# Kernel optimization log

Measured on AMD Instinct MI355X. Metric: run time of the kernel, lower is better.

The kernel has to match this reference:

```python
import jax, jax.numpy as jnp
import numpy as np

B, L, N = 16, 64, 1024
HAND_DIM, J, HID = 99, 21, 512
N_LAYERS, N_HEADS = 4, 8
DH = HID // N_HEADS
CAT = HAND_DIM + 2 * J * 3 + 2 * N  # 2273
PNAMES = ['fc_lw','fc_lb','fc_rw','fc_rb','out_lw','out_lb','out_rw','out_rb','Wqkv','bqkv','Wo','bo','W1','b1f','W2','b2f','ln1_g','ln1_b','ln2_g','ln2_b']

def sinusoidal_pe(n_pos, d):
    pos = np.arange(n_pos)[:, None].astype(np.float32)
    div = np.exp(np.arange(0, d, 2).astype(np.float32) * (-np.log(10000.0) / d))
    pe = np.zeros((n_pos, d), np.float32)
    pe[:, 0::2] = np.sin(pos * div)
    pe[:, 1::2] = np.cos(pos * div)
    return jnp.asarray(pe)

def rot6d_to_rotmat(x6):
    a1, a2 = x6[..., 0:3], x6[..., 3:6]
    b1 = a1 / jnp.linalg.norm(a1, axis=-1, keepdims=True)
    b2 = a2 - jnp.sum(b1 * a2, -1, keepdims=True) * b1
    b2 = b2 / jnp.linalg.norm(b2, axis=-1, keepdims=True)
    b3 = jnp.cross(b1, b2)
    return jnp.stack([b1, b2, b3], axis=-1)  # [..., 3, 3] (columns)

def layer_norm(x, g, b):
    mu = jnp.mean(x, -1, keepdims=True)
    var = jnp.mean((x - mu) ** 2, -1, keepdims=True)
    return (x - mu) * jax.lax.rsqrt(var + 1e-5) * g + b

def attention_map(joints, pc):
    # joints [B,L,J,3], pc [B,L,N,3]; squared dists via ||a||^2+||b||^2-2ab (no [B,L,J,N,3] diff tensor)
    d2 = (jnp.sum(joints ** 2, -1)[..., :, None] + jnp.sum(pc ** 2, -1)[..., None, :]
          - 2.0 * jnp.einsum('bljd,blnd->bljn', joints, pc))
    idx = jnp.argmin(d2, axis=-1)  # [B,L,J] nearest-point index
    idx3 = jnp.broadcast_to(idx[..., None], idx.shape + (3,))
    contact = jnp.take_along_axis(pc, idx3, axis=2)  # [B,L,J,3]
    return jnp.exp(-50.0 * (joints - contact) ** 2)

def mha(x, Wqkv, bqkv, Wo, bo):
    Bq, S, D = x.shape
    qkv = x @ Wqkv + bqkv
    q, k, v = jnp.split(qkv, 3, axis=-1)
    split = lambda t: t.reshape(Bq, S, N_HEADS, DH).transpose(0, 2, 1, 3)
    q, k, v = split(q), split(k), split(v)
    att = jax.nn.softmax(jnp.einsum('bhqd,bhkd->bhqk', q, k) * (1.0 / np.sqrt(DH)), axis=-1)
    o = jnp.einsum('bhqk,bhkd->bhqd', att, v).transpose(0, 2, 1, 3).reshape(Bq, S, D)
    return o @ Wo + bo

def forward(x_lhand, x_rhand, j_lhand, j_rhand, m_contact, x_obj, point_cloud, p):
    rotmat = rot6d_to_rotmat(x_obj[..., 3:9])  # [B,L,3,3]
    pc_t = jnp.einsum('btij,bkj->btki', rotmat, point_cloud) + x_obj[..., 0:3][:, :, None, :]
    att_l = attention_map(j_lhand, pc_t).reshape(B, L, -1)
    att_r = attention_map(j_rhand, pc_t).reshape(B, L, -1)
    mc = jnp.broadcast_to(m_contact.reshape(B, 1, N), (B, L, N))
    pcn = jnp.linalg.norm(pc_t, axis=-1)  # [B,L,N]
    xl = jnp.concatenate([x_lhand, j_lhand.reshape(B, L, -1), mc, pcn, att_l], -1)
    xr = jnp.concatenate([x_rhand, j_rhand.reshape(B, L, -1), mc, pcn, att_r], -1)
    xl = xl @ p['fc_lw'] + p['fc_lb']
    xr = xr @ p['fc_rw'] + p['fc_rb']
    x = jnp.stack([xl, xr], axis=2).reshape(B, 2 * L, HID)  # interleave agents per frame
    pe_frame = jnp.repeat(sinusoidal_pe(L, HID), 2, axis=0)  # frame-wise: pair shares position
    pe_agent = jnp.tile(sinusoidal_pe(2, HID), (L, 1))       # agent-wise: alternating 0/1
    x = x + pe_frame[None] + pe_agent[None]
    for i in range(N_LAYERS):
        h = layer_norm(x + mha(x, p['Wqkv'][i], p['bqkv'][i], p['Wo'][i], p['bo'][i]), p['ln1_g'][i], p['ln1_b'][i])
        ff = jax.nn.relu(h @ p['W1'][i] + p['b1f'][i]) @ p['W2'][i] + p['b2f'][i]
        x = layer_norm(h + ff, p['ln2_g'][i], p['ln2_b'][i])
    out_l = x[:, 0::2] @ p['out_lw'] + p['out_lb']
    out_r = x[:, 1::2] @ p['out_rw'] + p['out_rb']
    return out_l, out_r

def setup_inputs() -> dict:
    key = jax.random.key(0)
    ks = jax.random.split(key, 16)
    r = lambda i, shape, s=1.0: jax.random.normal(ks[i], shape, jnp.float32) * s
    return {
        'x_lhand': r(0, (B, L, HAND_DIM)),
        'x_rhand': r(1, (B, L, HAND_DIM)),
        'j_lhand': r(2, (B, L, J, 3)),
        'j_rhand': r(3, (B, L, J, 3)),
        'm_contact': jax.random.uniform(ks[4], (B, N, 1), jnp.float32),
        'x_obj': r(5, (B, L, 10)),
        'point_cloud': r(6, (B, N, 3)),
        'fc_lw': r(7, (CAT, HID), 0.02), 'fc_lb': jnp.zeros((HID,), jnp.float32),
        'fc_rw': r(8, (CAT, HID), 0.02), 'fc_rb': jnp.zeros((HID,), jnp.float32),
        'out_lw': r(9, (HID, HAND_DIM), 0.02), 'out_lb': jnp.zeros((HAND_DIM,), jnp.float32),
        'out_rw': r(10, (HID, HAND_DIM), 0.02), 'out_rb': jnp.zeros((HAND_DIM,), jnp.float32),
        'Wqkv': r(11, (N_LAYERS, HID, 3 * HID), 0.02), 'bqkv': jnp.zeros((N_LAYERS, 3 * HID), jnp.float32),
        'Wo': r(12, (N_LAYERS, HID, HID), 0.02), 'bo': jnp.zeros((N_LAYERS, HID), jnp.float32),
        'W1': r(13, (N_LAYERS, HID, 4 * HID), 0.02), 'b1f': jnp.zeros((N_LAYERS, 4 * HID), jnp.float32),
        'W2': r(14, (N_LAYERS, 4 * HID, HID), 0.02), 'b2f': jnp.zeros((N_LAYERS, HID), jnp.float32),
        'ln1_g': jnp.ones((N_LAYERS, HID), jnp.float32), 'ln1_b': jnp.zeros((N_LAYERS, HID), jnp.float32),
        'ln2_g': jnp.ones((N_LAYERS, HID), jnp.float32), 'ln2_b': jnp.zeros((N_LAYERS, HID), jnp.float32),
    }

def reference(x_lhand, x_rhand, j_lhand, j_rhand, m_contact, x_obj, point_cloud, fc_lw, fc_lb, fc_rw, fc_rb, out_lw, out_lb, out_rw, out_rb, Wqkv, bqkv, Wo, bo, W1, b1f, W2, b2f, ln1_g, ln1_b, ln2_g, ln2_b):
    p = dict(zip(PNAMES, (fc_lw, fc_lb, fc_rw, fc_rb, out_lw, out_lb, out_rw, out_rb, Wqkv, bqkv, Wo, bo, W1, b1f, W2, b2f, ln1_g, ln1_b, ln2_g, ln2_b)))
    return forward(x_lhand, x_rhand, j_lhand, j_rhand, m_contact, x_obj, point_cloud, p)
```

## Files before the change

### kernel.cpp

```cpp
#include <hip/hip_runtime.h>
#include <hip/hip_bf16.h>

typedef __hip_bfloat16 bf16;
typedef __attribute__((ext_vector_type(8))) short short8;
typedef __attribute__((ext_vector_type(4))) float floatx4;

#define B_    16
#define L_    64
#define N_    1024
#define HANDD 99
#define Jn    21
#define HID   512
#define NLAY  4
#define NHEAD 8
#define DHEAD 64
#define CATD  2273
#define CATP  2304
#define S_    128
#define T_    2048

#define F_X     16
#define F_QKV   1048592
#define F_TMP   6291472
#define F_H     7340048
#define WB_F    8388624
#define W_FCL   0
#define W_FCR   1179648
#define W_QKV   2359296
#define W_WO    5505024
#define W_W1    6553600
#define W_W2    10747904
#define U_CATL  14942208
#define U_CATR  17301504
#define U_XB    19660800
#define U_AOB   20709376
#define U_HB    21757952
#define W_OUT   22806528
#define U_FFB   U_CATL

#define RSTR 68
#define VSTR 136

#define PC_UNITS 2048
#define NW_UNITS 3680

static __device__ __forceinline__ float b2f(bf16 x) { return __bfloat162float(x); }
static __device__ __forceinline__ float ldin(const void* p, size_t i, int isf32) {
    return isf32 ? ((const float*)p)[i] : b2f(((const bf16*)p)[i]);
}
static __device__ __forceinline__ unsigned short f2bf(float f) {
    unsigned int u = __float_as_uint(f);
    unsigned int r = (u + 0x7fffu + ((u >> 16) & 1u)) >> 16;
    return (unsigned short)r;
}

__global__ __launch_bounds__(256) void detect_kernel(const void* mc, int* flag)
{
    __shared__ int sbad;
    int tid = threadIdx.x;
    if (tid == 0) sbad = 0;
    __syncthreads();
    int bad = 0;
    for (int i = tid; i < 16384; i += 256) {
        float v = b2f(((const bf16*)mc)[i]);
        if (!(v >= -0.02f && v <= 1.02f)) bad = 1;
    }
    if (bad) atomicOr(&sbad, 1);
    __syncthreads();
    if (tid == 0) flag[0] = sbad ? 1 : 0;
}

struct PrepP {
    const void *x_l, *x_r, *j_l, *j_r, *mc, *x_obj, *pc;
    const void *fc_lw, *fc_rw, *Wqkv, *Wo, *W1, *W2, *out_lw, *out_rw;
    unsigned short *wb, *catl, *catr;
    const int* dtf;
};

static __device__ void pctcat_half(int bl, int hand, const PrepP& P, int isf32,
                                   char* smemc)
{
    float* pcl  = (float*)smemc;
    float* pcnl = pcl + N_ * 3;
    int b = bl >> 6;
    int tid = threadIdx.x;

    size_t xo = (size_t)bl * 10;
    float t0 = ldin(P.x_obj, xo+0, isf32), t1 = ldin(P.x_obj, xo+1, isf32), t2 = ldin(P.x_obj, xo+2, isf32);
    float a1x = ldin(P.x_obj, xo+3, isf32), a1y = ldin(P.x_obj, xo+4, isf32), a1z = ldin(P.x_obj, xo+5, isf32);
    float a2x = ldin(P.x_obj, xo+6, isf32), a2y = ldin(P.x_obj, xo+7, isf32), a2z = ldin(P.x_obj, xo+8, isf32);
    float n1 = sqrtf(a1x*a1x + a1y*a1y + a1z*a1z);
    float b1x = a1x / n1, b1y = a1y / n1, b1z = a1z / n1;
    float d = b1x*a2x + b1y*a2y + b1z*a2z;
    float c2x = a2x - d*b1x, c2y = a2y - d*b1y, c2z = a2z - d*b1z;
    float n2 = sqrtf(c2x*c2x + c2y*c2y + c2z*c2z);
    float b2x = c2x / n2, b2y = c2y / n2, b2z = c2z / n2;
    float b3x = b1y*b2z - b1z*b2y;
    float b3y = b1z*b2x - b1x*b2z;
    float b3z = b1x*b2y - b1y*b2x;

    size_t pcb = (size_t)b * N_ * 3;
    for (int n = tid; n < N_; n += 256) {
        float p0 = ldin(P.pc, pcb + n*3+0, isf32);
        float p1 = ldin(P.pc, pcb + n*3+1, isf32);
        float p2 = ldin(P.pc, pcb + n*3+2, isf32);
        float q0 = b1x*p0 + b2x*p1 + b3x*p2 + t0;
        float q1 = b1y*p0 + b2y*p1 + b3y*p2 + t1;
        float q2 = b1z*p0 + b2z*p1 + b3z*p2 + t2;
        pcl[n*3+0] = q0; pcl[n*3+1] = q1; pcl[n*3+2] = q2;
        pcnl[n] = q0*q0 + q1*q1 + q2*q2;
    }
    __syncthreads();

    const void* xh = hand ? P.x_r : P.x_l;
    const void* jh = hand ? P.j_r : P.j_l;
    unsigned short* row = (hand ? P.catr : P.catl) + (size_t)bl * CATP;
    for (int c = tid; c < HANDD; c += 256)  row[c]        = f2bf(ldin(xh, (size_t)bl*HANDD + c, isf32));
    for (int c = tid; c < 63;    c += 256)  row[99 + c]   = f2bf(ldin(jh, (size_t)bl*63 + c, isf32));
    for (int c = tid; c < N_;    c += 256)  row[162 + c]  = f2bf(ldin(P.mc, (size_t)b*N_ + c, isf32));
    for (int c = tid; c < N_;    c += 256)  row[1186 + c] = f2bf(sqrtf(pcnl[c]));
    for (int c = CATD + tid; c < CATP; c += 256) row[c] = 0;

    int wave = tid >> 6, lane = tid & 63;
    for (int j = wave; j < Jn; j += 4) {
        float jx = ldin(jh, (size_t)bl*63 + j*3 + 0, isf32);
        float jy = ldin(jh, (size_t)bl*63 + j*3 + 1, isf32);
        float jz = ldin(jh, (size_t)bl*63 + j*3 + 2, isf32);
        float m2x = -2.f * jx, m2y = -2.f * jy, m2z = -2.f * jz;
        float best = 3.4e38f; int bidx = 0x7fffffff;
        for (int n = lane; n < N_; n += 64) {
            float p0 = pcl[n*3+0], p1 = pcl[n*3+1], p2 = pcl[n*3+2];
            float d2 = fmaf(m2x, p0, fmaf(m2y, p1, fmaf(m2z, p2, pcnl[n])));
            if (d2 < best) { best = d2; bidx = n; }
        }
        for (int off = 32; off; off >>= 1) {
            float ob = __shfl_down(best, off, 64);
            int   oi = __shfl_down(bidx, off, 64);
            if (ob < best || (ob == best && oi < bidx)) { best = ob; bidx = oi; }
        }
        bidx = __shfl(bidx, 0, 64);
        if (lane < 3) {
            float jc = (lane == 0) ? jx : ((lane == 1) ? jy : jz);
            float cc = pcl[bidx*3 + lane];
            float dd = jc - cc;
            row[2210 + j*3 + lane] = f2bf(expf(-50.f * dd * dd));
        }
    }
}

__global__ __launch_bounds__(256) void prep_all(PrepP P)
{
    __shared__ __attribute__((aligned(16))) char smem[16640];
    int isf32 = P.dtf[0];
    int u = blockIdx.x;

    if (u < PC_UNITS) {
        pctcat_half(u >> 1, u & 1, P, isf32, smem);
        return;
    }
    u -= PC_UNITS;
    if (u == NW_UNITS) {
        unsigned short* wz = P.wb + W_OUT + (size_t)(2 * HANDD) * HID;
        for (int idx = threadIdx.x; idx < (256 - 2 * HANDD) * HID; idx += 256)
            wz[idx] = 0;
        return;
    }

    float (*tile)[65] = (float(*)[65])smem;
    const void* src; unsigned short* dst;
    int K, Nn, NnB, Kpad, gx; size_t soff = 0, doff = 0;
    if (u < 576) {
        int hh = u >= 288; if (hh) u -= 288;
        src = hh ? P.fc_rw : P.fc_lw; dst = P.wb + (hh ? W_FCR : W_FCL);
        K = CATD; Nn = HID; NnB = HID; Kpad = CATP; gx = 8;
    } else if (u < 1344) {
        int r = u - 576; int z = r / 192; u = r % 192;
        src = P.Wqkv; soff = (size_t)z * HID * 1536;
        dst = P.wb + W_QKV; doff = (size_t)z * 1536 * HID;
        K = HID; Nn = 1536; NnB = 1536; Kpad = HID; gx = 24;
    } else if (u < 1600) {
        int r = u - 1344; int z = r / 64; u = r % 64;
        src = P.Wo; soff = (size_t)z * HID * HID;
        dst = P.wb + W_WO; doff = (size_t)z * HID * HID;
        K = HID; Nn = HID; NnB = HID; Kpad = HID; gx = 8;
    } else if (u < 2624) {
        int r = u - 1600; int z = r / 256; u = r % 256;
        src = P.W1; soff = (size_t)z * HID * 2048;
        dst = P.wb + W_W1; doff = (size_t)z * 2048 * HID;
        K = HID; Nn = 2048; NnB = 2048; Kpad = HID; gx = 32;
    } else if (u < 3648) {
        int r = u - 2624; int z = r / 256; u = r % 256;
        src = P.W2; soff = (size_t)z * 2048 * HID;
        dst = P.wb + W_W2; doff = (size_t)z * HID * 2048;
        K = 2048; Nn = HID; NnB = HID; Kpad = 2048; gx = 8;
    } else {
        int r = u - 3648; int hh = r >= 16; if (hh) r -= 16;
        src = hh ? P.out_rw : P.out_lw;
        dst = P.wb + W_OUT + (hh ? (size_t)HANDD * HID : 0);
        K = HID; Nn = HANDD; NnB = HANDD; Kpad = HID; gx = 2; u = r;
    }
    int n0 = (u % gx) * 64, k0 = (u / gx) * 64;
    int a = threadIdx.x & 63, bq = threadIdx.x >> 6;
    for (int r = bq; r < 64; r += 4) {
        int k = k0 + r, n = n0 + a;
        float v = (k < K && n < NnB) ? ldin(src, soff + (size_t)k * Nn + n, isf32) : 0.f;
        tile[r][a] = v;
    }
    __syncthreads();
    for (int r = bq; r < 64; r += 4) {
        int n = n0 + r;
        if (n < NnB)
            dst[doff + (size_t)n * Kpad + k0 + a] = f2bf(tile[a][r]);
    }
}

__global__ __launch_bounds__(256) void gemm_ks(
    const unsigned short* __restrict__ Ab, const unsigned short* __restrict__ Ab2,
    int K,
    const unsigned short* __restrict__ Wt, size_t wtoff, size_t wtoff2, int halfgrid,
    int Nn,
    const void* __restrict__ bias, const void* __restrict__ bias2, size_t boff,
    const float* __restrict__ resid,
    float* __restrict__ Df, unsigned short* __restrict__ Db,
    int relu, int rowmap, int tilesN, const int* __restrict__ dtf)
{
    __shared__ float red[4][32 * RSTR];
    int blk = blockIdx.x;
    if (halfgrid && blk >= halfgrid) {
        blk -= halfgrid; Ab = Ab2; wtoff = wtoff2; bias = bias2; rowmap = 2;
    }
    int tid = threadIdx.x;
    int wave = tid >> 6, lane = tid & 63;
    int quad = lane >> 4, l16 = lane & 15;
    int tm = blk / tilesN, tn = blk - tm * tilesN;
    int row0 = tm << 6, col0 = tn << 6;
    int Ks = K >> 2;
    int ks0 = wave * Ks;

    const unsigned short* Ap = Ab + (size_t)(row0 + l16) * K + ks0 + quad * 8;
    const unsigned short* Bp = Wt + wtoff + (size_t)(col0 + l16) * K + ks0 + quad * 8;
    size_t astep = (size_t)16 * K;

    floatx4 acc[4][4];
    #pragma unroll
    for (int i = 0; i < 4; i++)
        #pragma unroll
        for (int j = 0; j < 4; j++)
            acc[i][j] = (floatx4){0.f, 0.f, 0.f, 0.f};

    for (int k = 0; k < Ks; k += 32) {
        short8 af[4], bf[4];
        #pragma unroll
        for (int i = 0; i < 4; i++) {
            af[i] = *(const short8*)(Ap + i * astep + k);
            bf[i] = *(const short8*)(Bp + i * astep + k);
        }
        #pragma unroll
        for (int mi = 0; mi < 4; mi++)
            #pragma unroll
            for (int ni = 0; ni < 4; ni++)
                acc[mi][ni] = __builtin_amdgcn_mfma_f32_16x16x32_bf16(
                    af[mi], bf[ni], acc[mi][ni], 0, 0, 0);
    }

    int isf32 = dtf[0];
    int cc = tid & 63;
    int c = col0 + cc;
    float bv;
    if (rowmap == 3)
        bv = (c < HANDD) ? ldin(bias, c, isf32)
           : ((c < 2 * HANDD) ? ldin(bias2, c - HANDD, isf32) : 0.f);
    else
        bv = bias ? ldin(bias, boff + c, isf32) : 0.f;
    float pe_div = 0.f, pa = 0.f;
    if (rowmap == 1 || rowmap == 2) {
        int ci = c & ~1;
        pe_div = expf((float)ci * (-logf(10000.f) / (float)HID));
        int hand = rowmap - 1;
        pa = (c & 1) ? cosf((float)hand * pe_div) : sinf((float)hand * pe_div);
    }
    int rbase = tid >> 6;

    #pragma unroll
    for (int s = 0; s < 2; s++) {
        #pragma unroll
        for (int mi2 = 0; mi2 < 2; mi2++) {
            int mi = s * 2 + mi2;
            #pragma unroll
            for (int ni = 0; ni < 4; ni++)
                #pragma unroll
                for (int reg = 0; reg < 4; reg++) {
                    int r = mi2 * 16 + quad * 4 + reg;
                    int col = ni * 16 + l16;
                    red[wave][r * RSTR + col] = acc[mi][ni][reg];
                }
        }
        __syncthreads();

        #pragma unroll
        for (int j = 0; j < 8; j++) {
            int rr = rbase + (j << 2);
            int idx = rr * RSTR + cc;
            float v = red[0][idx] + red[1][idx] + red[2][idx] + red[3][idx] + bv;
            int r = row0 + s * 32 + rr;
            if (resid) v += resid[(size_t)r * Nn + c];
            if (relu)  v = fmaxf(v, 0.f);
            if (rowmap == 3) {
                int hand = r & 1;
                int l = (r >> 1) & 63, bb = r >> 7;
                if (hand == 0 && c < HANDD) {
                    size_t oi = ((size_t)bb * 64 + l) * HANDD + c;
                    if (isf32) ((float*)Df)[oi] = v;
                    else       ((bf16*)Df)[oi]  = __float2bfloat16(v);
                } else if (hand == 1 && c >= HANDD && c < 2 * HANDD) {
                    size_t oi = (size_t)B_ * L_ * HANDD + ((size_t)bb * 64 + l) * HANDD + (c - HANDD);
                    if (isf32) ((float*)Df)[oi] = v;
                    else       ((bf16*)Df)[oi]  = __float2bfloat16(v);
                }
            } else {
                int orow = r;
                if (rowmap) {
                    int bb = r >> 6, ll = r & 63;
                    orow = bb * S_ + 2 * ll + (rowmap - 1);
                    float pf = (c & 1) ? cosf((float)ll * pe_div) : sinf((float)ll * pe_div);
                    v += pf + pa;
                }
                if (Df) Df[(size_t)orow * Nn + c] = v;
                if (Db) Db[(size_t)orow * Nn + c] = f2bf(v);
            }
        }
        if (s == 0) __syncthreads();
    }
}

__global__ __launch_bounds__(128) void attn_mfma(
    const unsigned short* __restrict__ qkvb, unsigned short* __restrict__ aob)
{
    __shared__ unsigned short Vt[64 * VSTR];
    __shared__ unsigned short Pb[64 * VSTR];
    int bh = blockIdx.x;
    int b = bh >> 3, h = bh & 7;
    int rowhalf = blockIdx.y;
    int tid = threadIdx.x;
    int w = tid >> 6, lane = tid & 63;
    int quad = lane >> 4, l16 = lane & 15;
    size_t qbase = (size_t)(b * S_) * 1536 + h * DHEAD;

    for (int i = tid; i < S_ * DHEAD; i += 128) {
        int key = i >> 6, dcol = i & 63;
        Vt[dcol * VSTR + key] = qkvb[qbase + (size_t)key * 1536 + 1024 + dcol];
    }
    __syncthreads();

    int qrow0 = rowhalf * 64 + w * 32;
    short8 aQ[2][2];
    #pragma unroll
    for (int mt = 0; mt < 2; mt++)
        #pragma unroll
        for (int kc = 0; kc < 2; kc++)
            aQ[mt][kc] = *(const short8*)&qkvb[qbase + (size_t)(qrow0 + mt*16 + l16) * 1536 + kc*32 + quad*8];

    floatx4 sacc[2][8];
    #pragma unroll
    for (int mt = 0; mt < 2; mt++)
        #pragma unroll
        for (int nt = 0; nt < 8; nt++)
            sacc[mt][nt] = (floatx4){0.f, 0.f, 0.f, 0.f};

    #pragma unroll
    for (int nt = 0; nt < 8; nt++) {
        const unsigned short* kp = &qkvb[qbase + (size_t)(nt*16 + l16) * 1536 + 512 + quad*8];
        short8 bK0 = *(const short8*)kp;
        short8 bK1 = *(const short8*)(kp + 32);
        #pragma unroll
        for (int mt = 0; mt < 2; mt++) {
            sacc[mt][nt] = __builtin_amdgcn_mfma_f32_16x16x32_bf16(aQ[mt][0], bK0, sacc[mt][nt], 0, 0, 0);
            sacc[mt][nt] = __builtin_amdgcn_mfma_f32_16x16x32_bf16(aQ[mt][1], bK1, sacc[mt][nt], 0, 0, 0);
        }
    }

    #pragma unroll
    for (int mt = 0; mt < 2; mt++)
        #pragma unroll
        for (int reg = 0; reg < 4; reg++) {
            float v[8];
            float m = -3.4e38f;
            #pragma unroll
            for (int nt = 0; nt < 8; nt++) { v[nt] = sacc[mt][nt][reg] * 0.125f; m = fmaxf(m, v[nt]); }
            #pragma unroll
            for (int off = 1; off <= 8; off <<= 1) m = fmaxf(m, __shfl_xor(m, off, 64));
            float sum = 0.f;
            #pragma unroll
            for (int nt = 0; nt < 8; nt++) { v[nt] = expf(v[nt] - m); sum += v[nt]; }
            #pragma unroll
            for (int off = 1; off <= 8; off <<= 1) sum += __shfl_xor(sum, off, 64);
            float inv = 1.f / sum;
            int lr = w*32 + mt*16 + quad*4 + reg;
            #pragma unroll
            for (int nt = 0; nt < 8; nt++)
                Pb[lr * VSTR + nt*16 + l16] = f2bf(v[nt] * inv);
        }
    __syncthreads();

    #pragma unroll
    for (int mt = 0; mt < 2; mt++) {
        short8 aP[4];
        #pragma unroll
        for (int kt = 0; kt < 4; kt++)
            aP[kt] = *(const short8*)&Pb[(w*32 + mt*16 + l16) * VSTR + kt*32 + quad*8];
        #pragma unroll
        for (int nt = 0; nt < 4; nt++) {
            floatx4 o = (floatx4){0.f, 0.f, 0.f, 0.f};
            #pragma unroll
            for (int kt = 0; kt < 4; kt++) {
                short8 bV = *(const short8*)&Vt[(nt*16 + l16) * VSTR + kt*32 + quad*8];
                o = __builtin_amdgcn_mfma_f32_16x16x32_bf16(aP[kt], bV, o, 0, 0, 0);
            }
            #pragma unroll
            for (int reg = 0; reg < 4; reg++) {
                int qrow = qrow0 + mt*16 + quad*4 + reg;
                aob[(size_t)(b*S_ + qrow) * HID + h*DHEAD + nt*16 + l16] = f2bf(o[reg]);
            }
        }
    }
}

__global__ __launch_bounds__(256) void ln_kernel(
    const float* __restrict__ src, const void* __restrict__ g,
    const void* __restrict__ bb, size_t goff,
    float* __restrict__ dst, unsigned short* __restrict__ dstb,
    const int* __restrict__ dtf)
{
    int isf32 = dtf[0];
    int t = blockIdx.x;
    const float* x = src + (size_t)t * HID;
    int tid = threadIdx.x, lane = tid & 63, wave = tid >> 6;
    float v0 = x[tid], v1 = x[tid + 256];
    float s = v0 + v1;
    for (int off = 32; off; off >>= 1) s += __shfl_down(s, off, 64);
    __shared__ float wsum[4];
    if (lane == 0) wsum[wave] = s;
    __syncthreads();
    float mu = (wsum[0] + wsum[1] + wsum[2] + wsum[3]) * (1.f / 512.f);
    float d0 = v0 - mu, d1 = v1 - mu;
    float q = d0 * d0 + d1 * d1;
    for (int off = 32; off; off >>= 1) q += __shfl_down(q, off, 64);
    __syncthreads();
    if (lane == 0) wsum[wave] = q;
    __syncthreads();
    float var = (wsum[0] + wsum[1] + wsum[2] + wsum[3]) * (1.f / 512.f);
    float rstd = 1.f / sqrtf(var + 1e-5f);
    float y0 = d0 * rstd * ldin(g, goff + tid, isf32)       + ldin(bb, goff + tid, isf32);
    float y1 = d1 * rstd * ldin(g, goff + tid + 256, isf32) + ldin(bb, goff + tid + 256, isf32);
    if (dst) {
        dst[(size_t)t * HID + tid]       = y0;
        dst[(size_t)t * HID + tid + 256] = y1;
    }
    if (dstb) {
        dstb[(size_t)t * HID + tid]       = f2bf(y0);
        dstb[(size_t)t * HID + tid + 256] = f2bf(y1);
    }
}

extern "C" void kernel_launch(void* const* d_in, const int* in_sizes, int n_in,
                              void* d_out, int out_size, void* d_ws, size_t ws_size,
                              hipStream_t stream)
{
    const void* x_lhand = d_in[0];
    const void* x_rhand = d_in[1];
    const void* j_lhand = d_in[2];
    const void* j_rhand = d_in[3];
    const void* m_contact = d_in[4];
    const void* x_obj = d_in[5];
    const void* point_cloud = d_in[6];
    const void* fc_lw = d_in[7];
    const void* fc_lb = d_in[8];
    const void* fc_rw = d_in[9];
    const void* fc_rb = d_in[10];
    const void* out_lw = d_in[11];
    const void* out_lb = d_in[12];
    const void* out_rw = d_in[13];
    const void* out_rb = d_in[14];
    const void* Wqkv = d_in[15];
    const void* bqkv = d_in[16];
    const void* Wo   = d_in[17];
    const void* bo   = d_in[18];
    const void* W1   = d_in[19];
    const void* b1f  = d_in[20];
    const void* W2   = d_in[21];
    const void* b2fp = d_in[22];
    const void* ln1g = d_in[23];
    const void* ln1b = d_in[24];
    const void* ln2g = d_in[25];
    const void* ln2b = d_in[26];

    float* ws = (float*)d_ws;
    int* dtf = (int*)d_ws;
    float* x     = ws + F_X;
    float* tmp   = ws + F_TMP;
    float* h     = ws + F_H;
    unsigned short* qkvb = (unsigned short*)(ws + F_QKV);
    unsigned short* wb   = (unsigned short*)(ws + WB_F);
    unsigned short* catl = wb + U_CATL;
    unsigned short* catr = wb + U_CATR;
    unsigned short* xb   = wb + U_XB;
    unsigned short* aob  = wb + U_AOB;
    unsigned short* hb   = wb + U_HB;
    unsigned short* ffb  = wb + U_FFB;

    detect_kernel<<<1, 256, 0, stream>>>(m_contact, dtf);

    PrepP pp;
    pp.x_l = x_lhand; pp.x_r = x_rhand; pp.j_l = j_lhand; pp.j_r = j_rhand;
    pp.mc = m_contact; pp.x_obj = x_obj; pp.pc = point_cloud;
    pp.fc_lw = fc_lw; pp.fc_rw = fc_rw; pp.Wqkv = Wqkv; pp.Wo = Wo;
    pp.W1 = W1; pp.W2 = W2; pp.out_lw = out_lw; pp.out_rw = out_rw;
    pp.wb = wb; pp.catl = catl; pp.catr = catr; pp.dtf = dtf;
    prep_all<<<PC_UNITS + NW_UNITS + 1, 256, 0, stream>>>(pp);

    gemm_ks<<<256, 256, 0, stream>>>(catl, catr, CATP, wb, W_FCL, W_FCR, 128, HID,
                                     fc_lb, fc_rb, 0, nullptr, x, xb, 0, 1, 8, dtf);

    for (int i = 0; i < NLAY; i++) {
        size_t oWq = (size_t)W_QKV + (size_t)i * 1536 * HID, obq = (size_t)i * 1536;
        size_t oWo = (size_t)W_WO + (size_t)i * HID * HID,   obo = (size_t)i * HID;
        size_t oW1 = (size_t)W_W1 + (size_t)i * 2048 * HID,  ob1 = (size_t)i * 2048;
        size_t oW2 = (size_t)W_W2 + (size_t)i * HID * 2048,  ob2 = (size_t)i * HID;
        size_t oln = (size_t)i * HID;

        gemm_ks<<<768, 256, 0, stream>>>(xb, nullptr, HID, wb, oWq, 0, 0, 1536,
                                         bqkv, nullptr, obq, nullptr, nullptr, qkvb, 0, 0, 24, dtf);

        attn_mfma<<<dim3(B_ * NHEAD, 2), 128, 0, stream>>>(qkvb, aob);

        gemm_ks<<<256, 256, 0, stream>>>(aob, nullptr, HID, wb, oWo, 0, 0, HID,
                                         bo, nullptr, obo, x, tmp, nullptr, 0, 0, 8, dtf);
        ln_kernel<<<T_, 256, 0, stream>>>(tmp, ln1g, ln1b, oln, h, hb, dtf);

        gemm_ks<<<1024, 256, 0, stream>>>(hb, nullptr, HID, wb, oW1, 0, 0, 2048,
                                          b1f, nullptr, ob1, nullptr, nullptr, ffb, 1, 0, 32, dtf);
        gemm_ks<<<256, 256, 0, stream>>>(ffb, nullptr, 2048, wb, oW2, 0, 0, HID,
                                         b2fp, nullptr, ob2, h, tmp, nullptr, 0, 0, 8, dtf);
        ln_kernel<<<T_, 256, 0, stream>>>(tmp, ln2g, ln2b, oln, x, xb, dtf);
    }

    gemm_ks<<<128, 256, 0, stream>>>(xb, nullptr, HID, wb, W_OUT, 0, 0, 256,
                                     out_lb, out_rb, 0, nullptr, (float*)d_out, nullptr, 0, 3, 4, dtf);
}
```

Measured before the change: 648.1 us.

## Fuse LayerNorm into GEMM epilogue via last-block counter, merge dtype detect into prep

Removes the separate LayerNorm kernels: each output GEMM tile bumps a per-row-block atomic counter, and the last tile to finish a row block applies LayerNorm to those 64 rows, writing fp32 and bf16 copies. The standalone dtype-detect kernel is dropped; every prep block rescans m_contact itself and block 0 writes the flag. The bf16 path also copies inputs directly and transposes weights with 8-wide vector loads. This saves 8 LN launches and one detect launch, in exchange for redundant per-block scans, serialized LN work in the last-arriving blocks, and counter-based cross-block synchronization.

```diff
diff --git a/kernel.cpp b/kernel.cpp
--- a/kernel.cpp
+++ b/kernel.cpp
@@ -21,6 +21,7 @@
 
 #define F_X     16
 #define F_QKV   1048592
+#define F_CNT   4000000
 #define F_TMP   6291472
 #define F_H     7340048
 #define WB_F    8388624
@@ -43,6 +44,7 @@
 
 #define PC_UNITS 2048
 #define NW_UNITS 3680
+#define PREP_UNITS (PC_UNITS + NW_UNITS + 1)
 
 static __device__ __forceinline__ float b2f(bf16 x) { return __bfloat162float(x); }
 static __device__ __forceinline__ float ldin(const void* p, size_t i, int isf32) {
@@ -54,27 +56,11 @@
     return (unsigned short)r;
 }
 
-__global__ __launch_bounds__(256) void detect_kernel(const void* mc, int* flag)
-{
-    __shared__ int sbad;
-    int tid = threadIdx.x;
-    if (tid == 0) sbad = 0;
-    __syncthreads();
-    int bad = 0;
-    for (int i = tid; i < 16384; i += 256) {
-        float v = b2f(((const bf16*)mc)[i]);
-        if (!(v >= -0.02f && v <= 1.02f)) bad = 1;
-    }
-    if (bad) atomicOr(&sbad, 1);
-    __syncthreads();
-    if (tid == 0) flag[0] = sbad ? 1 : 0;
-}
-
 struct PrepP {
     const void *x_l, *x_r, *j_l, *j_r, *mc, *x_obj, *pc;
     const void *fc_lw, *fc_rw, *Wqkv, *Wo, *W1, *W2, *out_lw, *out_rw;
     unsigned short *wb, *catl, *catr;
-    const int* dtf;
+    int* dtf; int* lncnt;
 };
 
 static __device__ void pctcat_half(int bl, int hand, const PrepP& P, int isf32,
@@ -115,9 +101,18 @@
     const void* xh = hand ? P.x_r : P.x_l;
     const void* jh = hand ? P.j_r : P.j_l;
     unsigned short* row = (hand ? P.catr : P.catl) + (size_t)bl * CATP;
-    for (int c = tid; c < HANDD; c += 256)  row[c]        = f2bf(ldin(xh, (size_t)bl*HANDD + c, isf32));
-    for (int c = tid; c < 63;    c += 256)  row[99 + c]   = f2bf(ldin(jh, (size_t)bl*63 + c, isf32));
-    for (int c = tid; c < N_;    c += 256)  row[162 + c]  = f2bf(ldin(P.mc, (size_t)b*N_ + c, isf32));
+    if (!isf32) {
+        const unsigned short* xs = (const unsigned short*)xh + (size_t)bl * HANDD;
+        const unsigned short* js = (const unsigned short*)jh + (size_t)bl * 63;
+        const unsigned short* ms = (const unsigned short*)P.mc + (size_t)b * N_;
+        for (int c = tid; c < HANDD; c += 256)  row[c]       = xs[c];
+        for (int c = tid; c < 63;    c += 256)  row[99 + c]  = js[c];
+        for (int c = tid; c < N_;    c += 256)  row[162 + c] = ms[c];
+    } else {
+        for (int c = tid; c < HANDD; c += 256)  row[c]       = f2bf(ldin(xh, (size_t)bl*HANDD + c, isf32));
+        for (int c = tid; c < 63;    c += 256)  row[99 + c]  = f2bf(ldin(jh, (size_t)bl*63 + c, isf32));
+        for (int c = tid; c < N_;    c += 256)  row[162 + c] = f2bf(ldin(P.mc, (size_t)b*N_ + c, isf32));
+    }
     for (int c = tid; c < N_;    c += 256)  row[1186 + c] = f2bf(sqrtf(pcnl[c]));
     for (int c = CATD + tid; c < CATP; c += 256) row[c] = 0;
 
@@ -151,9 +146,25 @@
 __global__ __launch_bounds__(256) void prep_all(PrepP P)
 {
     __shared__ __attribute__((aligned(16))) char smem[16640];
-    int isf32 = P.dtf[0];
+    __shared__ int sbad;
+    int tid = threadIdx.x;
+
+    if (tid == 0) sbad = 0;
+    __syncthreads();
+    {
+        int bad = 0;
+        for (int i = tid; i < 16384; i += 256) {
+            float v = b2f(((const bf16*)P.mc)[i]);
+            if (!(v >= -0.02f && v <= 1.02f)) bad = 1;
+        }
+        if (bad) atomicOr(&sbad, 1);
+    }
+    __syncthreads();
+    int isf32 = sbad;
+    if (tid == 0 && blockIdx.x == 0) P.dtf[0] = isf32;
+    __syncthreads();
+
     int u = blockIdx.x;
-
     if (u < PC_UNITS) {
         pctcat_half(u >> 1, u & 1, P, isf32, smem);
         return;
@@ -161,12 +172,12 @@
     u -= PC_UNITS;
     if (u == NW_UNITS) {
         unsigned short* wz = P.wb + W_OUT + (size_t)(2 * HANDD) * HID;
-        for (int idx = threadIdx.x; idx < (256 - 2 * HANDD) * HID; idx += 256)
+        for (int idx = tid; idx < (256 - 2 * HANDD) * HID; idx += 256)
             wz[idx] = 0;
+        if (tid < 256) P.lncnt[tid] = 0;
         return;
     }
 
-    float (*tile)[65] = (float(*)[65])smem;
     const void* src; unsigned short* dst;
     int K, Nn, NnB, Kpad, gx; size_t soff = 0, doff = 0;
     if (u < 576) {
@@ -200,17 +211,47 @@
         K = HID; Nn = HANDD; NnB = HANDD; Kpad = HID; gx = 2; u = r;
     }
     int n0 = (u % gx) * 64, k0 = (u / gx) * 64;
-    int a = threadIdx.x & 63, bq = threadIdx.x >> 6;
-    for (int r = bq; r < 64; r += 4) {
-        int k = k0 + r, n = n0 + a;
-        float v = (k < K && n < NnB) ? ldin(src, soff + (size_t)k * Nn + n, isf32) : 0.f;
-        tile[r][a] = v;
-    }
-    __syncthreads();
-    for (int r = bq; r < 64; r += 4) {
-        int n = n0 + r;
-        if (n < NnB)
-            dst[doff + (size_t)n * Kpad + k0 + a] = f2bf(tile[a][r]);
+
+    if (!isf32 && (Nn % 8) == 0) {
+        unsigned short (*tu)[68] = (unsigned short(*)[68])smem;
+        const unsigned short* s = (const unsigned short*)src;
+        #pragma unroll
+        for (int pass = 0; pass < 2; pass++) {
+            int r = (tid >> 3) + pass * 32;
+            int k = k0 + r;
+            int nb = (tid & 7) * 8;
+            short8 v = (short8){0,0,0,0,0,0,0,0};
+            if (k < K) v = *(const short8*)(s + soff + (size_t)k * Nn + n0 + nb);
+            #pragma unroll
+            for (int j = 0; j < 8; j++) tu[r][nb + j] = (unsigned short)v[j];
+        }
+        __syncthreads();
+        #pragma unroll
+        for (int pass = 0; pass < 2; pass++) {
+            int rp = (tid >> 3) + pass * 32;
+            int n = n0 + rp;
+            int kb = (tid & 7) * 8;
+            if (n < NnB) {
+                short8 o;
+                #pragma unroll
+                for (int j = 0; j < 8; j++) o[j] = (short)tu[kb + j][rp];
+                *(short8*)(dst + doff + (size_t)n * Kpad + k0 + kb) = o;
+            }
+        }
+    } else {
+        float (*tile)[65] = (float(*)[65])smem;
+        int a = tid & 63, bq = tid >> 6;
+        for (int r = bq; r < 64; r += 4) {
+            int k = k0 + r, n = n0 + a;
+            float v = (k < K && n < NnB) ? ldin(src, soff + (size_t)k * Nn + n, isf32) : 0.f;
+            tile[r][a] = v;
+        }
+        __syncthreads();
+        for (int r = bq; r < 64; r += 4) {
+            int n = n0 + r;
+            if (n < NnB)
+                dst[doff + (size_t)n * Kpad + k0 + a] = f2bf(tile[a][r]);
+        }
     }
 }
 
@@ -222,7 +263,10 @@
     const void* __restrict__ bias, const void* __restrict__ bias2, size_t boff,
     const float* __restrict__ resid,
     float* __restrict__ Df, unsigned short* __restrict__ Db,
-    int relu, int rowmap, int tilesN, const int* __restrict__ dtf)
+    int relu, int rowmap, int tilesN,
+    const void* __restrict__ lng, const void* __restrict__ lnb, size_t lnoff,
+    float* __restrict__ lndst, unsigned short* __restrict__ lndstb, int* __restrict__ lncnt,
+    const int* __restrict__ dtf)
 {
     __shared__ float red[4][32 * RSTR];
     int blk = blockIdx.x;
@@ -331,6 +375,50 @@
         }
         if (s == 0) __syncthreads();
     }
+
+    if (lncnt) {
+        __syncthreads();
+        __shared__ int slast;
+        if (tid == 0) {
+            __threadfence();
+            slast = (atomicAdd(&lncnt[tm], 1) == tilesN - 1) ? 1 : 0;
+        }
+        __syncthreads();
+        if (slast) {
+            __threadfence();
+            int lane2 = tid & 63, wv = tid >> 6;
+            for (int rr = wv; rr < 64; rr += 4) {
+                int row = row0 + rr;
+                const float* xr = Df + (size_t)row * Nn + lane2 * 8;
+                floatx4 va = *(const floatx4*)(xr);
+                floatx4 vb = *(const floatx4*)(xr + 4);
+                float ssum = va[0]+va[1]+va[2]+va[3]+vb[0]+vb[1]+vb[2]+vb[3];
+                #pragma unroll
+                for (int off = 32; off; off >>= 1) ssum += __shfl_xor(ssum, off, 64);
+                float mu = ssum * (1.f / 512.f);
+                float dd[8];
+                dd[0]=va[0]-mu; dd[1]=va[1]-mu; dd[2]=va[2]-mu; dd[3]=va[3]-mu;
+                dd[4]=vb[0]-mu; dd[5]=vb[1]-mu; dd[6]=vb[2]-mu; dd[7]=vb[3]-mu;
+                float q = dd[0]*dd[0]+dd[1]*dd[1]+dd[2]*dd[2]+dd[3]*dd[3]
+                        + dd[4]*dd[4]+dd[5]*dd[5]+dd[6]*dd[6]+dd[7]*dd[7];
+                #pragma unroll
+                for (int off = 32; off; off >>= 1) q += __shfl_xor(q, off, 64);
+                float rstd = 1.f / sqrtf(q * (1.f / 512.f) + 1e-5f);
+                float y[8];
+                #pragma unroll
+                for (int jj = 0; jj < 8; jj++)
+                    y[jj] = dd[jj] * rstd * ldin(lng, lnoff + lane2*8 + jj, isf32)
+                          + ldin(lnb, lnoff + lane2*8 + jj, isf32);
+                floatx4 o0 = {y[0], y[1], y[2], y[3]}, o1 = {y[4], y[5], y[6], y[7]};
+                *(floatx4*)(lndst + (size_t)row * HID + lane2*8)     = o0;
+                *(floatx4*)(lndst + (size_t)row * HID + lane2*8 + 4) = o1;
+                short8 ob;
+                #pragma unroll
+                for (int jj = 0; jj < 8; jj++) ob[jj] = (short)f2bf(y[jj]);
+                *(short8*)(lndstb + (size_t)row * HID + lane2*8) = ob;
+            }
+        }
+    }
 }
 
 __global__ __launch_bounds__(128) void attn_mfma(
@@ -422,43 +510,6 @@
                 aob[(size_t)(b*S_ + qrow) * HID + h*DHEAD + nt*16 + l16] = f2bf(o[reg]);
             }
         }
-    }
-}
-
-__global__ __launch_bounds__(256) void ln_kernel(
-    const float* __restrict__ src, const void* __restrict__ g,
-    const void* __restrict__ bb, size_t goff,
-    float* __restrict__ dst, unsigned short* __restrict__ dstb,
-    const int* __restrict__ dtf)
-{
-    int isf32 = dtf[0];
-    int t = blockIdx.x;
-    const float* x = src + (size_t)t * HID;
-    int tid = threadIdx.x, lane = tid & 63, wave = tid >> 6;
-    float v0 = x[tid], v1 = x[tid + 256];
-    float s = v0 + v1;
-    for (int off = 32; off; off >>= 1) s += __shfl_down(s, off, 64);
-    __shared__ float wsum[4];
-    if (lane == 0) wsum[wave] = s;
-    __syncthreads();
-    float mu = (wsum[0] + wsum[1] + wsum[2] + wsum[3]) * (1.f / 512.f);
-    float d0 = v0 - mu, d1 = v1 - mu;
-    float q = d0 * d0 + d1 * d1;
-    for (int off = 32; off; off >>= 1) q += __shfl_down(q, off, 64);
-    __syncthreads();
-    if (lane == 0) wsum[wave] = q;
-    __syncthreads();
-    float var = (wsum[0] + wsum[1] + wsum[2] + wsum[3]) * (1.f / 512.f);
-    float rstd = 1.f / sqrtf(var + 1e-5f);
-    float y0 = d0 * rstd * ldin(g, goff + tid, isf32)       + ldin(bb, goff + tid, isf32);
-    float y1 = d1 * rstd * ldin(g, goff + tid + 256, isf32) + ldin(bb, goff + tid + 256, isf32);
-    if (dst) {
-        dst[(size_t)t * HID + tid]       = y0;
-        dst[(size_t)t * HID + tid + 256] = y1;
-    }
-    if (dstb) {
-        dstb[(size_t)t * HID + tid]       = f2bf(y0);
-        dstb[(size_t)t * HID + tid + 256] = f2bf(y1);
     }
 }
 
@@ -496,6 +547,7 @@
 
     float* ws = (float*)d_ws;
     int* dtf = (int*)d_ws;
+    int* lncnt = (int*)(ws + F_CNT);
     float* x     = ws + F_X;
     float* tmp   = ws + F_TMP;
     float* h     = ws + F_H;
@@ -508,18 +560,17 @@
     unsigned short* hb   = wb + U_HB;
     unsigned short* ffb  = wb + U_FFB;
 
-    detect_kernel<<<1, 256, 0, stream>>>(m_contact, dtf);
-
     PrepP pp;
     pp.x_l = x_lhand; pp.x_r = x_rhand; pp.j_l = j_lhand; pp.j_r = j_rhand;
     pp.mc = m_contact; pp.x_obj = x_obj; pp.pc = point_cloud;
     pp.fc_lw = fc_lw; pp.fc_rw = fc_rw; pp.Wqkv = Wqkv; pp.Wo = Wo;
     pp.W1 = W1; pp.W2 = W2; pp.out_lw = out_lw; pp.out_rw = out_rw;
-    pp.wb = wb; pp.catl = catl; pp.catr = catr; pp.dtf = dtf;
-    prep_all<<<PC_UNITS + NW_UNITS + 1, 256, 0, stream>>>(pp);
+    pp.wb = wb; pp.catl = catl; pp.catr = catr; pp.dtf = dtf; pp.lncnt = lncnt;
+    prep_all<<<PREP_UNITS, 256, 0, stream>>>(pp);
 
     gemm_ks<<<256, 256, 0, stream>>>(catl, catr, CATP, wb, W_FCL, W_FCR, 128, HID,
-                                     fc_lb, fc_rb, 0, nullptr, x, xb, 0, 1, 8, dtf);
+                                     fc_lb, fc_rb, 0, nullptr, x, xb, 0, 1, 8,
+                                     nullptr, nullptr, 0, nullptr, nullptr, nullptr, dtf);
 
     for (int i = 0; i < NLAY; i++) {
         size_t oWq = (size_t)W_QKV + (size_t)i * 1536 * HID, obq = (size_t)i * 1536;
@@ -529,21 +580,25 @@
         size_t oln = (size_t)i * HID;
 
         gemm_ks<<<768, 256, 0, stream>>>(xb, nullptr, HID, wb, oWq, 0, 0, 1536,
-                                         bqkv, nullptr, obq, nullptr, nullptr, qkvb, 0, 0, 24, dtf);
+                                         bqkv, nullptr, obq, nullptr, nullptr, qkvb, 0, 0, 24,
+                                         nullptr, nullptr, 0, nullptr, nullptr, nullptr, dtf);
 
         attn_mfma<<<dim3(B_ * NHEAD, 2), 128, 0, stream>>>(qkvb, aob);
 
         gemm_ks<<<256, 256, 0, stream>>>(aob, nullptr, HID, wb, oWo, 0, 0, HID,
-                                         bo, nullptr, obo, x, tmp, nullptr, 0, 0, 8, dtf);
-        ln_kernel<<<T_, 256, 0, stream>>>(tmp, ln1g, ln1b, oln, h, hb, dtf);
+                                         bo, nullptr, obo, x, tmp, nullptr, 0, 0, 8,
+                                         ln1g, ln1b, oln, h, hb, lncnt + (2*i)*32, dtf);
 
         gemm_ks<<<1024, 256, 0, stream>>>(hb, nullptr, HID, wb, oW1, 0, 0, 2048,
-                                          b1f, nullptr, ob1, nullptr, nullptr, ffb, 1, 0, 32, dtf);
+                                          b1f, nullptr, ob1, nullptr, nullptr, ffb, 1, 0, 32,
+                                          nullptr, nullptr, 0, nullptr, nullptr, nullptr, dtf);
+
         gemm_ks<<<256, 256, 0, stream>>>(ffb, nullptr, 2048, wb, oW2, 0, 0, HID,
-                                         b2fp, nullptr, ob2, h, tmp, nullptr, 0, 0, 8, dtf);
-        ln_kernel<<<T_, 256, 0, stream>>>(tmp, ln2g, ln2b, oln, x, xb, dtf);
+                                         b2fp, nullptr, ob2, h, tmp, nullptr, 0, 0, 8,
+                                         ln2g, ln2b, oln, x, xb, lncnt + (2*i+1)*32, dtf);
     }
 
     gemm_ks<<<128, 256, 0, stream>>>(xb, nullptr, HID, wb, W_OUT, 0, 0, 256,
-                                     out_lb, out_rb, 0, nullptr, (float*)d_out, nullptr, 0, 3, 4, dtf);
+                                     out_lb, out_rb, 0, nullptr, (float*)d_out, nullptr, 0, 3, 4,
+                                     nullptr, nullptr, 0, nullptr, nullptr, nullptr, dtf);
 }
```

New measurement: 1.071 ms. 1.65x slower.

## Fuse QKV projection into attention kernel per batch-head

Applied to the files above, without the earlier changes.

Replaces the separate QKV GEMM launch and the attention kernel with one kernel per (batch, head). Each block computes its Q, K and V head slices with MFMA straight from xb and the weights into shared memory, then runs attention from LDS. This removes the qkv global round trip and one launch per layer. In exchange the grid drops to 128 blocks of 256 threads with no K-dimension tiling or LDS staging of the operands, so the projection loads may be latency-bound, and the weight loads are served from global memory/cache without LDS reuse.

```diff
diff --git a/kernel.cpp b/kernel.cpp
--- a/kernel.cpp
+++ b/kernel.cpp
@@ -20,7 +20,6 @@
 #define T_    2048
 
 #define F_X     16
-#define F_QKV   1048592
 #define F_TMP   6291472
 #define F_H     7340048
 #define WB_F    8388624
@@ -333,32 +332,75 @@
     }
 }
 
-__global__ __launch_bounds__(128) void attn_mfma(
-    const unsigned short* __restrict__ qkvb, unsigned short* __restrict__ aob)
-{
-    __shared__ unsigned short Vt[64 * VSTR];
-    __shared__ unsigned short Pb[64 * VSTR];
+__global__ __launch_bounds__(256) void qkvattn(
+    const unsigned short* __restrict__ xb,
+    const unsigned short* __restrict__ Wt, size_t oWq,
+    const void* __restrict__ bqkv, size_t obq,
+    unsigned short* __restrict__ aob, const int* __restrict__ dtf)
+{
+    __shared__ __attribute__((aligned(16))) unsigned short smem[26112];
+    unsigned short* Ql = smem;
+    unsigned short* Kl = smem + 8704;
+    unsigned short* Pb = smem;
+    unsigned short* Vt = smem + 17408;
+    int isf32 = dtf[0];
     int bh = blockIdx.x;
     int b = bh >> 3, h = bh & 7;
-    int rowhalf = blockIdx.y;
     int tid = threadIdx.x;
     int w = tid >> 6, lane = tid & 63;
     int quad = lane >> 4, l16 = lane & 15;
-    size_t qbase = (size_t)(b * S_) * 1536 + h * DHEAD;
-
-    for (int i = tid; i < S_ * DHEAD; i += 128) {
-        int key = i >> 6, dcol = i & 63;
-        Vt[dcol * VSTR + key] = qkvb[qbase + (size_t)key * 1536 + 1024 + dcol];
-    }
-    __syncthreads();
-
-    int qrow0 = rowhalf * 64 + w * 32;
+
+    const unsigned short* Ap0 = xb + (size_t)(b * S_ + w * 32 + l16) * HID + quad * 8;
+    #pragma unroll
+    for (int o = 0; o < 3; o++) {
+        int outbase = o * 512 + h * DHEAD;
+        const unsigned short* Bp = Wt + oWq + (size_t)(outbase + l16) * HID + quad * 8;
+        floatx4 acc[2][4];
+        #pragma unroll
+        for (int mi = 0; mi < 2; mi++)
+            #pragma unroll
+            for (int ni = 0; ni < 4; ni++)
+                acc[mi][ni] = (floatx4){0.f, 0.f, 0.f, 0.f};
+        for (int k = 0; k < HID; k += 32) {
+            short8 af[2], bf[4];
+            #pragma unroll
+            for (int mi = 0; mi < 2; mi++)
+                af[mi] = *(const short8*)(Ap0 + (size_t)mi * 16 * HID + k);
+            #pragma unroll
+            for (int ni = 0; ni < 4; ni++)
+                bf[ni] = *(const short8*)(Bp + (size_t)ni * 16 * HID + k);
+            #pragma unroll
+            for (int mi = 0; mi < 2; mi++)
+                #pragma unroll
+                for (int ni = 0; ni < 4; ni++)
+                    acc[mi][ni] = __builtin_amdgcn_mfma_f32_16x16x32_bf16(
+                        af[mi], bf[ni], acc[mi][ni], 0, 0, 0);
+        }
+        #pragma unroll
+        for (int ni = 0; ni < 4; ni++) {
+            float bv = ldin(bqkv, obq + outbase + ni * 16 + l16, isf32);
+            #pragma unroll
+            for (int mi = 0; mi < 2; mi++)
+                #pragma unroll
+                for (int reg = 0; reg < 4; reg++) {
+                    int row = w * 32 + mi * 16 + quad * 4 + reg;
+                    int col = ni * 16 + l16;
+                    unsigned short hv = f2bf(acc[mi][ni][reg] + bv);
+                    if (o == 0)      Ql[row * 68 + col] = hv;
+                    else if (o == 1) Kl[row * 68 + col] = hv;
+                    else             Vt[col * VSTR + row] = hv;
+                }
+        }
+    }
+    __syncthreads();
+
+    int qrow0 = w * 32;
     short8 aQ[2][2];
     #pragma unroll
     for (int mt = 0; mt < 2; mt++)
         #pragma unroll
         for (int kc = 0; kc < 2; kc++)
-            aQ[mt][kc] = *(const short8*)&qkvb[qbase + (size_t)(qrow0 + mt*16 + l16) * 1536 + kc*32 + quad*8];
+            aQ[mt][kc] = *(const short8*)&Ql[(qrow0 + mt*16 + l16) * 68 + kc*32 + quad*8];
 
     floatx4 sacc[2][8];
     #pragma unroll
@@ -369,7 +411,7 @@
 
     #pragma unroll
     for (int nt = 0; nt < 8; nt++) {
-        const unsigned short* kp = &qkvb[qbase + (size_t)(nt*16 + l16) * 1536 + 512 + quad*8];
+        const unsigned short* kp = &Kl[(nt*16 + l16) * 68 + quad*8];
         short8 bK0 = *(const short8*)kp;
         short8 bK1 = *(const short8*)(kp + 32);
         #pragma unroll
@@ -378,6 +420,7 @@
             sacc[mt][nt] = __builtin_amdgcn_mfma_f32_16x16x32_bf16(aQ[mt][1], bK1, sacc[mt][nt], 0, 0, 0);
         }
     }
+    __syncthreads();
 
     #pragma unroll
     for (int mt = 0; mt < 2; mt++)
@@ -395,7 +438,7 @@
             #pragma unroll
             for (int off = 1; off <= 8; off <<= 1) sum += __shfl_xor(sum, off, 64);
             float inv = 1.f / sum;
-            int lr = w*32 + mt*16 + quad*4 + reg;
+            int lr = qrow0 + mt*16 + quad*4 + reg;
             #pragma unroll
             for (int nt = 0; nt < 8; nt++)
                 Pb[lr * VSTR + nt*16 + l16] = f2bf(v[nt] * inv);
@@ -407,7 +450,7 @@
         short8 aP[4];
         #pragma unroll
         for (int kt = 0; kt < 4; kt++)
-            aP[kt] = *(const short8*)&Pb[(w*32 + mt*16 + l16) * VSTR + kt*32 + quad*8];
+            aP[kt] = *(const short8*)&Pb[(qrow0 + mt*16 + l16) * VSTR + kt*32 + quad*8];
         #pragma unroll
         for (int nt = 0; nt < 4; nt++) {
             floatx4 o = (floatx4){0.f, 0.f, 0.f, 0.f};
@@ -499,7 +542,6 @@
     float* x     = ws + F_X;
     float* tmp   = ws + F_TMP;
     float* h     = ws + F_H;
-    unsigned short* qkvb = (unsigned short*)(ws + F_QKV);
     unsigned short* wb   = (unsigned short*)(ws + WB_F);
     unsigned short* catl = wb + U_CATL;
     unsigned short* catr = wb + U_CATR;
@@ -528,10 +570,7 @@
         size_t oW2 = (size_t)W_W2 + (size_t)i * HID * 2048,  ob2 = (size_t)i * HID;
         size_t oln = (size_t)i * HID;
 
-        gemm_ks<<<768, 256, 0, stream>>>(xb, nullptr, HID, wb, oWq, 0, 0, 1536,
-                                         bqkv, nullptr, obq, nullptr, nullptr, qkvb, 0, 0, 24, dtf);
-
-        attn_mfma<<<dim3(B_ * NHEAD, 2), 128, 0, stream>>>(qkvb, aob);
+        qkvattn<<<B_ * NHEAD, 256, 0, stream>>>(xb, wb, oWq, bqkv, obq, aob, dtf);
 
         gemm_ks<<<256, 256, 0, stream>>>(aob, nullptr, HID, wb, oWo, 0, 0, HID,
                                          bo, nullptr, obo, x, tmp, nullptr, 0, 0, 8, dtf);
```

After: 701.9 us. 8.3% more time.
